# Optimization experiments

Hardware: AMD Instinct MI355X
Metric: run time of the kernel (lower is better)

## Reference

```python
import jax, jax.numpy as jnp
import numpy as np

N = 25600          # total nodes
B = 64             # graphs in batch
NPG = N // B       # nodes per graph (400)
K = 16             # in-degree (regular graph)
E = N * K          # edges
D = 128            # hidden dim = out dim
L = 4              # DGN layers
NUM_ATOM = 128


def _linear_init(key, out_s, in_s):
    lim = 1.0 / np.sqrt(in_s)
    return jax.random.uniform(key, (out_s, in_s), jnp.float32, -lim, lim)


def setup_inputs() -> dict:
    key = jax.random.key(0)
    ks = jax.random.split(key, 16)
    node_feat = jax.random.randint(ks[0], (N,), 0, NUM_ATOM)
    # K-regular in-degree graph, edges intra-graph; dst sorted
    dst = jnp.repeat(jnp.arange(N), K)                       # [E]
    src_local = jax.random.randint(ks[1], (E,), 0, NPG)
    src = (dst // NPG) * NPG + src_local                     # same graph as dst
    eig = jax.random.normal(ks[2], (E, 2), jnp.float32)
    snorm_n = jnp.full((N, 1), 1.0 / np.sqrt(NPG), jnp.float32)
    graph_ids = jnp.arange(N) // NPG
    emb = jax.random.normal(ks[3], (NUM_ATOM, D), jnp.float32) * 0.02
    pre_W = jnp.stack([_linear_init(jax.random.fold_in(ks[4], i), D, 2 * D) for i in range(L)])
    pre_b = jnp.zeros((L, D), jnp.float32)
    post_W = jnp.stack([_linear_init(jax.random.fold_in(ks[5], i), D, 5 * D) for i in range(L)])
    post_b = jnp.zeros((L, D), jnp.float32)
    r_W0 = _linear_init(ks[6], 64, 128); r_b0 = jnp.zeros((64,), jnp.float32)
    r_W1 = _linear_init(ks[7], 32, 64);  r_b1 = jnp.zeros((32,), jnp.float32)
    r_W2 = _linear_init(ks[8], 128, 32); r_b2 = jnp.zeros((128,), jnp.float32)
    return dict(node_feat=node_feat, src=src, dst=dst, eig=eig, snorm_n=snorm_n,
                graph_ids=graph_ids, emb=emb, pre_W=pre_W, pre_b=pre_b,
                post_W=post_W, post_b=post_b, r_W0=r_W0, r_b0=r_b0,
                r_W1=r_W1, r_b1=r_b1, r_W2=r_W2, r_b2=r_b2)


def _dgn_layer(h, src, dst, eig, snorm_n, Wp, bp, Wq, bq):
    n = h.shape[0]
    # pretrans on edges: Linear(cat(h_src, h_dst))  [E, D]
    z2 = jnp.concatenate([h[src], h[dst]], axis=-1)
    e = jnp.einsum('ei,oi->eo', z2, Wp) + bp
    seg_sum = lambda v: jax.ops.segment_sum(v, dst, num_segments=n, indices_are_sorted=True)
    s = seg_sum(e)
    mean = s / K
    mx = jax.ops.segment_max(e, dst, num_segments=n, indices_are_sorted=True)
    # directional aggregator (eig_idx=1)
    w = eig[:, 1]
    denom = seg_sum(jnp.abs(w)) + 1e-8                       # [n]
    ew = w / denom[dst]                                      # [E]
    dir_agg = jnp.abs(seg_sum(e * ew[:, None]) - seg_sum(ew)[:, None] * h)
    agg = jnp.concatenate([h, mean, s, mx, dir_agg], axis=-1)  # [n, 5D]
    hn = jnp.einsum('ni,oi->no', agg, Wq) + bq
    hn = hn * snorm_n           # graph_norm
    hn = jax.nn.relu(hn)
    return h + hn               # residual (in_dim == out_dim)


def reference(node_feat, src, dst, eig, snorm_n, graph_ids, emb,
              pre_W, pre_b, post_W, post_b,
              r_W0, r_b0, r_W1, r_b1, r_W2, r_b2):
    h = emb[node_feat]                                       # AtomEncoder
    for i in range(L):
        h = _dgn_layer(h, src, dst, eig, snorm_n, pre_W[i], pre_b[i], post_W[i], post_b[i])
    # mean_nodes per graph (equal-sized graphs)
    hg = jax.ops.segment_sum(h, graph_ids, num_segments=B, indices_are_sorted=True) / NPG
    y = jax.nn.relu(hg @ r_W0.T + r_b0)
    y = jax.nn.relu(y @ r_W1.T + r_b1)
    return y @ r_W2.T + r_b2                                 # [B, 128]
```

## Files before the change

kernel.cpp:

```cpp
#include <hip/hip_runtime.h>
#include <cstddef>

#define NN 25600
#define BB 64
#define NPG 400
#define KK 16
#define LL 4

typedef _Float16 half_t;
typedef _Float16 h8 __attribute__((ext_vector_type(8)));
typedef _Float16 h4 __attribute__((ext_vector_type(4)));
typedef _Float16 h2 __attribute__((ext_vector_type(2)));
typedef float f32x4 __attribute__((ext_vector_type(4)));

__global__ __launch_bounds__(256) void prep_k(const float* __restrict__ preW,
                                              const float* __restrict__ preb,
                                              const float* __restrict__ postW,
                                              half_t* __restrict__ WpreH,
                                              half_t* __restrict__ WpreL,
                                              float* __restrict__ bpre,
                                              half_t* __restrict__ WpostH,
                                              half_t* __restrict__ WpostL) {
  int idx = blockIdx.x * 256 + threadIdx.x;
  const int n1 = LL * 256 * 128;
  const int n2 = n1 + LL * 256;
  const int n3 = n2 + LL * 128 * 512;
  if (idx < n1) {
    int l = idx / 32768;
    int q = idx % 32768;
    int j = q & 7, lane = (q >> 3) & 63, kc = (q >> 9) & 3, c16 = q >> 11;
    int col = c16 * 16 + (lane & 15);
    int k = kc * 32 + (lane >> 4) * 8 + j;
    float v = (col < 128) ? preW[(size_t)l * 32768 + (size_t)col * 256 + k]
                          : preW[(size_t)l * 32768 + (size_t)(col - 128) * 256 + 128 + k];
    half_t hi = (half_t)v;
    WpreH[idx] = hi;
    WpreL[idx] = (half_t)(v - (float)hi);
  } else if (idx < n2) {
    int r = idx - n1;
    int l = r / 256, o = r % 256;
    bpre[r] = (o < 128) ? 0.f : preb[l * 128 + (o - 128)];
  } else if (idx < n3) {
    int r = idx - n2;
    int l = r / 65536;
    int q = r % 65536;
    int j = q & 7, lane = (q >> 3) & 63, kc = (q >> 9) & 15, c16 = q >> 13;
    int col = c16 * 16 + (lane & 15);
    int k = kc * 32 + (lane >> 4) * 8 + j;
    int jblk = k >> 7, kk = k & 127;
    const float* base = postW + (size_t)l * 128 * 640 + (size_t)col * 640;
    float v;
    if (jblk == 0)      v = base[kk];
    else if (jblk == 1) v = base[128 + kk] * (1.f / 16.f) + base[256 + kk];
    else if (jblk == 2) v = base[384 + kk];
    else                v = base[512 + kk];
    half_t hi = (half_t)v;
    WpostH[r] = hi;
    WpostL[r] = (half_t)(v - (float)hi);
  }
}

__global__ __launch_bounds__(256) void embed_k(const int* __restrict__ nf,
                                               const float* __restrict__ emb,
                                               half_t* __restrict__ Hh,
                                               half_t* __restrict__ Hl) {
  int idx = blockIdx.x * 256 + threadIdx.x;
  int n = idx >> 5;
  int d4 = idx & 31;
  int a = nf[n];
  float4 v = *(const float4*)(emb + (size_t)a * 128 + d4 * 4);
  h4 hi, lo;
  const float* vp = &v.x;
#pragma unroll
  for (int j = 0; j < 4; ++j) {
    half_t h = (half_t)vp[j];
    hi[j] = h;
    lo[j] = (half_t)(vp[j] - (float)h);
  }
  *(h4*)(Hh + (size_t)n * 128 + d4 * 4) = hi;
  *(h4*)(Hl + (size_t)n * 128 + d4 * 4) = lo;
}

__global__ __launch_bounds__(256) void pre_gemm_k(const half_t* __restrict__ Ah_g,
                                                  const half_t* __restrict__ Al_g,
                                                  const half_t* __restrict__ Wh_g,
                                                  const half_t* __restrict__ Wl_g,
                                                  float* __restrict__ preA) {
  __shared__ half_t Ahs[64][132];
  __shared__ half_t Als[64][132];
  const int tid = threadIdx.x;
  const int bid = blockIdx.x;
  const int swz = (bid & 7) * 50 + (bid >> 3);
  const int r0 = swz * 64;
  const int wid = tid >> 6, lane = tid & 63;
  const int wm = wid >> 1, wn = wid & 1;
  const int lr = lane & 15, lk = (lane >> 4) * 8;
  f32x4 acc[2][4] = {};

  {
    const int row = tid >> 2;
#pragma unroll
    for (int s = 0; s < 4; ++s) {
      const int koff = (tid & 3) * 8 + s * 32;
      const size_t g = (size_t)(r0 + row) * 128 + koff;
      *(h8*)&Ahs[row][koff] = *(const h8*)(Ah_g + g);
      *(h8*)&Als[row][koff] = *(const h8*)(Al_g + g);
    }
  }
  __syncthreads();

#pragma unroll
  for (int kc = 0; kc < 4; ++kc) {
    h8 af[2][2];
#pragma unroll
    for (int mi = 0; mi < 2; ++mi) {
      const int r = wm * 32 + mi * 16 + lr;
      af[mi][0] = *(const h8*)&Ahs[r][kc * 32 + lk];
      af[mi][1] = *(const h8*)&Als[r][kc * 32 + lk];
    }
#pragma unroll
    for (int nj = 0; nj < 4; ++nj) {
      const size_t fi = ((size_t)((wn * 4 + nj) * 4 + kc) * 64 + lane) * 8;
      const h8 b0v = *(const h8*)(Wh_g + fi);
      const h8 b1v = *(const h8*)(Wl_g + fi);
#pragma unroll
      for (int mi = 0; mi < 2; ++mi) {
        acc[mi][nj] = __builtin_amdgcn_mfma_f32_16x16x32_f16(af[mi][0], b0v, acc[mi][nj], 0, 0, 0);
        acc[mi][nj] = __builtin_amdgcn_mfma_f32_16x16x32_f16(af[mi][0], b1v, acc[mi][nj], 0, 0, 0);
        acc[mi][nj] = __builtin_amdgcn_mfma_f32_16x16x32_f16(af[mi][1], b0v, acc[mi][nj], 0, 0, 0);
      }
    }
  }
#pragma unroll
  for (int mi = 0; mi < 2; ++mi) {
    const int rowb = r0 + wm * 32 + mi * 16 + (lane >> 4) * 4;
#pragma unroll
    for (int nj = 0; nj < 4; ++nj) {
      const int col = wn * 64 + nj * 16 + lr;
#pragma unroll
      for (int q = 0; q < 4; ++q) {
        preA[(size_t)(rowb + q) * 128 + col] = acc[mi][nj][q];
      }
    }
  }
}

__global__ __launch_bounds__(256) void agg_post_k(const float* __restrict__ preA,
                                                  const int* __restrict__ src,
                                                  const float* __restrict__ eig,
                                                  const half_t* __restrict__ WpHg,
                                                  const half_t* __restrict__ WpLg,
                                                  const float* __restrict__ bpre128,
                                                  half_t* __restrict__ Hh,
                                                  half_t* __restrict__ Hl,
                                                  const half_t* __restrict__ Wh,
                                                  const half_t* __restrict__ Wl,
                                                  const float* __restrict__ bias,
                                                  const float* __restrict__ snorm) {
  __shared__ half_t Ah[16][392];
  __shared__ half_t Al[16][392];
  __shared__ float bsh[16][132];
  const int tid = threadIdx.x;
  const int bid = blockIdx.x;
  const int swz = (bid & 7) * 200 + (bid >> 3);
  const int r0 = swz * 16;
  const int wid = tid >> 6, lane = tid & 63;
  const int wn = wid;
  const int lr = lane & 15, lk = (lane >> 4) * 8;
  const int d0 = 2 * lane;

  const int frow = r0 + lr;
  h8 afh[4][2];
#pragma unroll
  for (int hc = 0; hc < 4; ++hc) {
    afh[hc][0] = *(const h8*)(Hh + (size_t)frow * 128 + hc * 32 + lk);
    afh[hc][1] = *(const h8*)(Hl + (size_t)frow * 128 + hc * 32 + lk);
  }

  {
    f32x4 bacc[2] = {};
#pragma unroll
    for (int kc = 0; kc < 4; ++kc) {
#pragma unroll
      for (int nj = 0; nj < 2; ++nj) {
        const size_t fi = ((size_t)((8 + wn * 2 + nj) * 4 + kc) * 64 + lane) * 8;
        const h8 b0v = *(const h8*)(WpHg + fi);
        const h8 b1v = *(const h8*)(WpLg + fi);
        bacc[nj] = __builtin_amdgcn_mfma_f32_16x16x32_f16(afh[kc][0], b0v, bacc[nj], 0, 0, 0);
        bacc[nj] = __builtin_amdgcn_mfma_f32_16x16x32_f16(afh[kc][0], b1v, bacc[nj], 0, 0, 0);
        bacc[nj] = __builtin_amdgcn_mfma_f32_16x16x32_f16(afh[kc][1], b0v, bacc[nj], 0, 0, 0);
      }
    }
    const int rowb = (lane >> 4) * 4;
#pragma unroll
    for (int nj = 0; nj < 2; ++nj) {
      const int col = (wn * 2 + nj) * 16 + lr;
      const float bv = bpre128[col];
#pragma unroll
      for (int q = 0; q < 4; ++q) {
        bsh[rowb + q][col] = bacc[nj][q] + bv;
      }
    }
  }
  __syncthreads();

  for (int i = 0; i < 4; ++i) {
    const int lrow = wid * 4 + i;
    const int n = r0 + lrow;
    int sv[KK];
    float wv[KK];
    {
      const int4* sp4 = (const int4*)(src + (size_t)n * KK);
      const float4* ep4 = (const float4*)(eig + (size_t)n * KK * 2);
#pragma unroll
      for (int t = 0; t < 4; ++t) {
        const int4 s4 = sp4[t];
        sv[4 * t + 0] = s4.x;
        sv[4 * t + 1] = s4.y;
        sv[4 * t + 2] = s4.z;
        sv[4 * t + 3] = s4.w;
      }
#pragma unroll
      for (int t = 0; t < 8; ++t) {
        const float4 e4 = ep4[t];
        wv[2 * t + 0] = e4.y;
        wv[2 * t + 1] = e4.w;
      }
    }
    float denom = 0.f;
#pragma unroll
    for (int e = 0; e < KK; ++e) denom += fabsf(wv[e]);
    denom += 1e-8f;
    const float inv = 1.f / denom;
    float sum_ew = 0.f;
#pragma unroll
    for (int e = 0; e < KK; ++e) {
      wv[e] *= inv;
      sum_ew += wv[e];
    }
    float sA0 = 0.f, sA1 = 0.f, wA0 = 0.f, wA1 = 0.f;
    float mA0 = -3.402823466e+38f, mA1 = -3.402823466e+38f;
#pragma unroll
    for (int e = 0; e < KK; ++e) {
      const float2 a = *(const float2*)(preA + (size_t)sv[e] * 128 + d0);
      sA0 += a.x;
      sA1 += a.y;
      wA0 = fmaf(wv[e], a.x, wA0);
      wA1 = fmaf(wv[e], a.y, wA1);
      mA0 = fmaxf(mA0, a.x);
      mA1 = fmaxf(mA1, a.y);
    }
    const float2 b = {bsh[lrow][d0], bsh[lrow][d0 + 1]};
    const h2 hh2 = *(const h2*)(Hh + (size_t)n * 128 + d0);
    const h2 hl2 = *(const h2*)(Hl + (size_t)n * 128 + d0);
    const float hx = (float)hh2[0] + (float)hl2[0];
    const float hy = (float)hh2[1] + (float)hl2[1];
    auto wr2 = [&](int kcol, float v0, float v1) {
      h2 hi, lo;
      hi[0] = (half_t)v0;
      hi[1] = (half_t)v1;
      lo[0] = (half_t)(v0 - (float)hi[0]);
      lo[1] = (half_t)(v1 - (float)hi[1]);
      *(h2*)&Ah[lrow][kcol] = hi;
      *(h2*)&Al[lrow][kcol] = lo;
    };
    wr2(d0, sA0 + 16.f * b.x, sA1 + 16.f * b.y);
    wr2(128 + d0, mA0 + b.x, mA1 + b.y);
    wr2(256 + d0, fabsf(wA0 + sum_ew * (b.x - hx)), fabsf(wA1 + sum_ew * (b.y - hy)));
  }
  __syncthreads();

  f32x4 acc[2] = {};
#pragma unroll
  for (int kc = 0; kc < 16; ++kc) {
    h8 a0, a1;
    if (kc < 4) {
      a0 = afh[kc & 3][0];
      a1 = afh[kc & 3][1];
    } else {
      a0 = *(const h8*)&Ah[lr][(kc - 4) * 32 + lk];
      a1 = *(const h8*)&Al[lr][(kc - 4) * 32 + lk];
    }
#pragma unroll
    for (int nj = 0; nj < 2; ++nj) {
      const size_t fi = ((size_t)((wn * 2 + nj) * 16 + kc) * 64 + lane) * 8;
      const h8 b0v = *(const h8*)(Wh + fi);
      const h8 b1v = *(const h8*)(Wl + fi);
      acc[nj] = __builtin_amdgcn_mfma_f32_16x16x32_f16(a0, b0v, acc[nj], 0, 0, 0);
      acc[nj] = __builtin_amdgcn_mfma_f32_16x16x32_f16(a0, b1v, acc[nj], 0, 0, 0);
      acc[nj] = __builtin_amdgcn_mfma_f32_16x16x32_f16(a1, b0v, acc[nj], 0, 0, 0);
    }
  }

  const int rowb = r0 + (lane >> 4) * 4;
#pragma unroll
  for (int nj = 0; nj < 2; ++nj) {
    const int col = wn * 32 + nj * 16 + lr;
    const float bv = bias[col];
#pragma unroll
    for (int q = 0; q < 4; ++q) {
      const int r = rowb + q;
      float a = acc[nj][q] + bv;
      a *= snorm[r];
      a = fmaxf(a, 0.f);
      const size_t off = (size_t)r * 128 + col;
      const float hold = (float)Hh[off] + (float)Hl[off];
      const float hn = hold + a;
      const half_t hi = (half_t)hn;
      Hh[off] = hi;
      Hl[off] = (half_t)(hn - (float)hi);
    }
  }
}

__global__ __launch_bounds__(256) void reduce_mlp_k(const half_t* __restrict__ Hh,
                                                    const half_t* __restrict__ Hl,
                                                    const float* __restrict__ W0, const float* __restrict__ b0,
                                                    const float* __restrict__ W1, const float* __restrict__ b1,
                                                    const float* __restrict__ W2, const float* __restrict__ b2,
                                                    float* __restrict__ out) {
  __shared__ float hgs[128];
  __shared__ float red[128];
  __shared__ float y0s[64];
  __shared__ float y1s[32];
  __shared__ float wb[64 * 130];
  const int g = blockIdx.x;
  const int t = threadIdx.x;
  {
    const int d = t & 127, hf = t >> 7;
    const size_t base = ((size_t)g * NPG + (size_t)hf * 200) * 128 + d;
    float acc = 0.f;
    for (int i = 0; i < 200; ++i) {
      const size_t off = base + (size_t)i * 128;
      acc += (float)Hh[off] + (float)Hl[off];
    }
    if (hf) red[d] = acc;
    __syncthreads();
    if (!hf) hgs[d] = (acc + red[d]) * (1.f / (float)NPG);
  }
  __syncthreads();
  for (int idx = t; idx < 64 * 128; idx += 256) {
    wb[(idx >> 7) * 130 + (idx & 127)] = W0[idx];
  }
  __syncthreads();
  if (t < 64) {
    float a = b0[t];
    const float* w = &wb[t * 130];
    for (int k = 0; k < 128; ++k) a = fmaf(hgs[k], w[k], a);
    y0s[t] = fmaxf(a, 0.f);
  }
  __syncthreads();
  for (int idx = t; idx < 32 * 64; idx += 256) {
    wb[(idx >> 6) * 66 + (idx & 63)] = W1[idx];
  }
  __syncthreads();
  if (t < 32) {
    float a = b1[t];
    const float* w = &wb[t * 66];
    for (int k = 0; k < 64; ++k) a = fmaf(y0s[k], w[k], a);
    y1s[t] = fmaxf(a, 0.f);
  }
  __syncthreads();
  for (int idx = t; idx < 128 * 32; idx += 256) {
    wb[(idx >> 5) * 34 + (idx & 31)] = W2[idx];
  }
  __syncthreads();
  if (t < 128) {
    float a = b2[t];
    const float* w = &wb[t * 34];
    for (int k = 0; k < 32; ++k) a = fmaf(y1s[k], w[k], a);
    out[(size_t)g * 128 + t] = a;
  }
}

extern "C" void kernel_launch(void* const* d_in, const int* in_sizes, int n_in,
                              void* d_out, int out_size, void* d_ws, size_t ws_size,
                              hipStream_t stream) {
  const int* node_feat = (const int*)d_in[0];
  const int* src = (const int*)d_in[1];
  const float* eig = (const float*)d_in[3];
  const float* snorm = (const float*)d_in[4];
  const float* emb = (const float*)d_in[6];
  const float* preW = (const float*)d_in[7];
  const float* preb = (const float*)d_in[8];
  const float* postW = (const float*)d_in[9];
  const float* postb = (const float*)d_in[10];
  const float* rW0 = (const float*)d_in[11];
  const float* rb0 = (const float*)d_in[12];
  const float* rW1 = (const float*)d_in[13];
  const float* rb1 = (const float*)d_in[14];
  const float* rW2 = (const float*)d_in[15];
  const float* rb2 = (const float*)d_in[16];
  float* out = (float*)d_out;

  half_t* Hh = (half_t*)d_ws;
  half_t* Hl = Hh + (size_t)NN * 128;
  float* preA = (float*)(Hl + (size_t)NN * 128);
  half_t* WpreH = (half_t*)(preA + (size_t)NN * 128);
  half_t* WpreL = WpreH + (size_t)LL * 32768;
  half_t* WpostH = WpreL + (size_t)LL * 32768;
  half_t* WpostL = WpostH + (size_t)LL * 65536;
  float* bpre = (float*)(WpostL + (size_t)LL * 65536);

  prep_k<<<1540, 256, 0, stream>>>(preW, preb, postW, WpreH, WpreL, bpre, WpostH, WpostL);
  embed_k<<<(NN * 32) / 256, 256, 0, stream>>>(node_feat, emb, Hh, Hl);

  for (int l = 0; l < LL; ++l) {
    pre_gemm_k<<<NN / 64, 256, 0, stream>>>(
        Hh, Hl, WpreH + (size_t)l * 32768, WpreL + (size_t)l * 32768, preA);
    agg_post_k<<<NN / 16, 256, 0, stream>>>(
        preA, src, eig,
        WpreH + (size_t)l * 32768, WpreL + (size_t)l * 32768,
        bpre + (size_t)l * 256 + 128,
        Hh, Hl,
        WpostH + (size_t)l * 65536, WpostL + (size_t)l * 65536,
        postb + (size_t)l * 128, snorm);
  }

  reduce_mlp_k<<<BB, 256, 0, stream>>>(Hh, Hl, rW0, rb0, rW1, rb1, rW2, rb2, out);
}
```

Measured before the change: 280.1 us.

## Double row tile in agg_post and stream neighbor gathers via global_load_lds

The aggregation+post-GEMM kernel now processes 32 rows per block instead of 16, so each weight fragment loaded from global memory is reused across two MFMA row tiles, and the grid is halved. The per-edge gather of preA rows is rewritten to use global_load_lds into a per-wave double-buffered LDS stage, with explicit vmcnt/lgkmcnt waits so the next pair of neighbor rows loads while the current pair is accumulated. This targets gather latency and weight-load traffic, at the cost of more LDS per block, more registers, fewer blocks, and fragile hand-written waitcnt ordering.

```diff
diff --git a/kernel.cpp b/kernel.cpp
--- a/kernel.cpp
+++ b/kernel.cpp
@@ -12,6 +12,9 @@
 typedef _Float16 h4 __attribute__((ext_vector_type(4)));
 typedef _Float16 h2 __attribute__((ext_vector_type(2)));
 typedef float f32x4 __attribute__((ext_vector_type(4)));
+
+#define GCAST(p) ((const __attribute__((address_space(1))) void*)(p))
+#define SCAST(p) ((__attribute__((address_space(3))) void*)(p))
 
 __global__ __launch_bounds__(256) void prep_k(const float* __restrict__ preW,
                                               const float* __restrict__ preb,
@@ -145,40 +148,46 @@
   }
 }
 
-__global__ __launch_bounds__(256) void agg_post_k(const float* __restrict__ preA,
-                                                  const int* __restrict__ src,
-                                                  const float* __restrict__ eig,
-                                                  const half_t* __restrict__ WpHg,
-                                                  const half_t* __restrict__ WpLg,
-                                                  const float* __restrict__ bpre128,
-                                                  half_t* __restrict__ Hh,
-                                                  half_t* __restrict__ Hl,
-                                                  const half_t* __restrict__ Wh,
-                                                  const half_t* __restrict__ Wl,
-                                                  const float* __restrict__ bias,
-                                                  const float* __restrict__ snorm) {
-  __shared__ half_t Ah[16][392];
-  __shared__ half_t Al[16][392];
-  __shared__ float bsh[16][132];
+__global__ __launch_bounds__(256, 2) void agg_post_k(const float* __restrict__ preA,
+                                                     const int* __restrict__ src,
+                                                     const float* __restrict__ eig,
+                                                     const half_t* __restrict__ WpHg,
+                                                     const half_t* __restrict__ WpLg,
+                                                     const float* __restrict__ bpre128,
+                                                     half_t* __restrict__ Hh,
+                                                     half_t* __restrict__ Hl,
+                                                     const half_t* __restrict__ Wh,
+                                                     const half_t* __restrict__ Wl,
+                                                     const float* __restrict__ bias,
+                                                     const float* __restrict__ snorm) {
+  __shared__ half_t Ah[32][392];
+  __shared__ half_t Al[32][392];
+  __shared__ float bsh[32][132];
+  __shared__ float stage[4][2][2][128];
   const int tid = threadIdx.x;
   const int bid = blockIdx.x;
-  const int swz = (bid & 7) * 200 + (bid >> 3);
-  const int r0 = swz * 16;
+  const int swz = (bid & 7) * 100 + (bid >> 3);
+  const int r0 = swz * 32;
   const int wid = tid >> 6, lane = tid & 63;
   const int wn = wid;
   const int lr = lane & 15, lk = (lane >> 4) * 8;
   const int d0 = 2 * lane;
-
-  const int frow = r0 + lr;
-  h8 afh[4][2];
-#pragma unroll
-  for (int hc = 0; hc < 4; ++hc) {
-    afh[hc][0] = *(const h8*)(Hh + (size_t)frow * 128 + hc * 32 + lk);
-    afh[hc][1] = *(const h8*)(Hl + (size_t)frow * 128 + hc * 32 + lk);
+  const int glane4 = (lane & 31) * 4;
+  const int gsel = lane >> 5;
+
+  h8 afh[2][4][2];
+#pragma unroll
+  for (int mi = 0; mi < 2; ++mi) {
+    const int frow = r0 + mi * 16 + lr;
+#pragma unroll
+    for (int hc = 0; hc < 4; ++hc) {
+      afh[mi][hc][0] = *(const h8*)(Hh + (size_t)frow * 128 + hc * 32 + lk);
+      afh[mi][hc][1] = *(const h8*)(Hl + (size_t)frow * 128 + hc * 32 + lk);
+    }
   }
 
   {
-    f32x4 bacc[2] = {};
+    f32x4 bacc[2][2] = {};
 #pragma unroll
     for (int kc = 0; kc < 4; ++kc) {
 #pragma unroll
@@ -186,26 +195,32 @@
         const size_t fi = ((size_t)((8 + wn * 2 + nj) * 4 + kc) * 64 + lane) * 8;
         const h8 b0v = *(const h8*)(WpHg + fi);
         const h8 b1v = *(const h8*)(WpLg + fi);
-        bacc[nj] = __builtin_amdgcn_mfma_f32_16x16x32_f16(afh[kc][0], b0v, bacc[nj], 0, 0, 0);
-        bacc[nj] = __builtin_amdgcn_mfma_f32_16x16x32_f16(afh[kc][0], b1v, bacc[nj], 0, 0, 0);
-        bacc[nj] = __builtin_amdgcn_mfma_f32_16x16x32_f16(afh[kc][1], b0v, bacc[nj], 0, 0, 0);
+#pragma unroll
+        for (int mi = 0; mi < 2; ++mi) {
+          bacc[mi][nj] = __builtin_amdgcn_mfma_f32_16x16x32_f16(afh[mi][kc][0], b0v, bacc[mi][nj], 0, 0, 0);
+          bacc[mi][nj] = __builtin_amdgcn_mfma_f32_16x16x32_f16(afh[mi][kc][0], b1v, bacc[mi][nj], 0, 0, 0);
+          bacc[mi][nj] = __builtin_amdgcn_mfma_f32_16x16x32_f16(afh[mi][kc][1], b0v, bacc[mi][nj], 0, 0, 0);
+        }
       }
     }
     const int rowb = (lane >> 4) * 4;
 #pragma unroll
-    for (int nj = 0; nj < 2; ++nj) {
-      const int col = (wn * 2 + nj) * 16 + lr;
-      const float bv = bpre128[col];
-#pragma unroll
-      for (int q = 0; q < 4; ++q) {
-        bsh[rowb + q][col] = bacc[nj][q] + bv;
-      }
-    }
-  }
-  __syncthreads();
-
-  for (int i = 0; i < 4; ++i) {
-    const int lrow = wid * 4 + i;
+    for (int mi = 0; mi < 2; ++mi) {
+#pragma unroll
+      for (int nj = 0; nj < 2; ++nj) {
+        const int col = (wn * 2 + nj) * 16 + lr;
+        const float bv = bpre128[col];
+#pragma unroll
+        for (int q = 0; q < 4; ++q) {
+          bsh[mi * 16 + rowb + q][col] = bacc[mi][nj][q] + bv;
+        }
+      }
+    }
+  }
+  __syncthreads();
+
+  for (int i = 0; i < 8; ++i) {
+    const int lrow = wid * 8 + i;
     const int n = r0 + lrow;
     int sv[KK];
     float wv[KK];
@@ -227,6 +242,14 @@
         wv[2 * t + 1] = e4.w;
       }
     }
+    const h2 hh2 = *(const h2*)(Hh + (size_t)n * 128 + d0);
+    const h2 hl2 = *(const h2*)(Hl + (size_t)n * 128 + d0);
+    const float hx = (float)hh2[0] + (float)hl2[0];
+    const float hy = (float)hh2[1] + (float)hl2[1];
+    const float bx = bsh[lrow][d0];
+    const float by = bsh[lrow][d0 + 1];
+    const float tbx = bx - hx;
+    const float tby = by - hy;
     float denom = 0.f;
 #pragma unroll
     for (int e = 0; e < KK; ++e) denom += fabsf(wv[e]);
@@ -238,23 +261,45 @@
       wv[e] *= inv;
       sum_ew += wv[e];
     }
-    float sA0 = 0.f, sA1 = 0.f, wA0 = 0.f, wA1 = 0.f;
-    float mA0 = -3.402823466e+38f, mA1 = -3.402823466e+38f;
-#pragma unroll
-    for (int e = 0; e < KK; ++e) {
-      const float2 a = *(const float2*)(preA + (size_t)sv[e] * 128 + d0);
-      sA0 += a.x;
-      sA1 += a.y;
-      wA0 = fmaf(wv[e], a.x, wA0);
-      wA1 = fmaf(wv[e], a.y, wA1);
-      mA0 = fmaxf(mA0, a.x);
-      mA1 = fmaxf(mA1, a.y);
-    }
-    const float2 b = {bsh[lrow][d0], bsh[lrow][d0 + 1]};
-    const h2 hh2 = *(const h2*)(Hh + (size_t)n * 128 + d0);
-    const h2 hl2 = *(const h2*)(Hl + (size_t)n * 128 + d0);
-    const float hx = (float)hh2[0] + (float)hl2[0];
-    const float hy = (float)hh2[1] + (float)hl2[1];
+    float sX = 0.f, sY = 0.f, wX = 0.f, wY = 0.f;
+    float mX = -3.402823466e+38f, mY = -3.402823466e+38f;
+
+#define ISSUE(c, buf)                                                              \
+    {                                                                              \
+      const float* gp = preA + (size_t)sv[2 * (c) + gsel] * 128 + glane4;          \
+      __builtin_amdgcn_global_load_lds(GCAST(gp), SCAST(&stage[wid][buf][0][0]),   \
+                                       16, 0, 0);                                  \
+    }
+#define ACCUM(c, buf)                                                              \
+    {                                                                              \
+      const float2 aA = *(const float2*)&stage[wid][buf][0][d0];                   \
+      const float2 aB = *(const float2*)&stage[wid][buf][1][d0];                   \
+      sX += aA.x; sY += aA.y;                                                      \
+      wX = fmaf(wv[2 * (c)], aA.x, wX); wY = fmaf(wv[2 * (c)], aA.y, wY);          \
+      mX = fmaxf(mX, aA.x); mY = fmaxf(mY, aA.y);                                  \
+      sX += aB.x; sY += aB.y;                                                      \
+      wX = fmaf(wv[2 * (c) + 1], aB.x, wX); wY = fmaf(wv[2 * (c) + 1], aB.y, wY);  \
+      mX = fmaxf(mX, aB.x); mY = fmaxf(mY, aB.y);                                  \
+    }
+#define WAITV1 asm volatile("s_waitcnt vmcnt(1)" ::: "memory");
+#define WAITV0 asm volatile("s_waitcnt vmcnt(0)" ::: "memory");
+#define LGKM0  asm volatile("s_waitcnt lgkmcnt(0)" ::: "memory");
+
+    ISSUE(0, 0) ISSUE(1, 1)
+    WAITV1 ACCUM(0, 0) LGKM0 ISSUE(2, 0)
+    WAITV1 ACCUM(1, 1) LGKM0 ISSUE(3, 1)
+    WAITV1 ACCUM(2, 0) LGKM0 ISSUE(4, 0)
+    WAITV1 ACCUM(3, 1) LGKM0 ISSUE(5, 1)
+    WAITV1 ACCUM(4, 0) LGKM0 ISSUE(6, 0)
+    WAITV1 ACCUM(5, 1) LGKM0 ISSUE(7, 1)
+    WAITV1 ACCUM(6, 0)
+    WAITV0 ACCUM(7, 1)
+#undef ISSUE
+#undef ACCUM
+#undef WAITV1
+#undef WAITV0
+#undef LGKM0
+
     auto wr2 = [&](int kcol, float v0, float v1) {
       h2 hi, lo;
       hi[0] = (half_t)v0;
@@ -264,51 +309,60 @@
       *(h2*)&Ah[lrow][kcol] = hi;
       *(h2*)&Al[lrow][kcol] = lo;
     };
-    wr2(d0, sA0 + 16.f * b.x, sA1 + 16.f * b.y);
-    wr2(128 + d0, mA0 + b.x, mA1 + b.y);
-    wr2(256 + d0, fabsf(wA0 + sum_ew * (b.x - hx)), fabsf(wA1 + sum_ew * (b.y - hy)));
-  }
-  __syncthreads();
-
-  f32x4 acc[2] = {};
+    wr2(d0, sX + 16.f * bx, sY + 16.f * by);
+    wr2(128 + d0, mX + bx, mY + by);
+    wr2(256 + d0, fabsf(wX + sum_ew * tbx), fabsf(wY + sum_ew * tby));
+  }
+  __syncthreads();
+
+  f32x4 acc[2][2] = {};
 #pragma unroll
   for (int kc = 0; kc < 16; ++kc) {
-    h8 a0, a1;
-    if (kc < 4) {
-      a0 = afh[kc & 3][0];
-      a1 = afh[kc & 3][1];
-    } else {
-      a0 = *(const h8*)&Ah[lr][(kc - 4) * 32 + lk];
-      a1 = *(const h8*)&Al[lr][(kc - 4) * 32 + lk];
+    h8 a0[2], a1[2];
+#pragma unroll
+    for (int mi = 0; mi < 2; ++mi) {
+      if (kc < 4) {
+        a0[mi] = afh[mi][kc & 3][0];
+        a1[mi] = afh[mi][kc & 3][1];
+      } else {
+        a0[mi] = *(const h8*)&Ah[mi * 16 + lr][(kc - 4) * 32 + lk];
+        a1[mi] = *(const h8*)&Al[mi * 16 + lr][(kc - 4) * 32 + lk];
+      }
     }
 #pragma unroll
     for (int nj = 0; nj < 2; ++nj) {
       const size_t fi = ((size_t)((wn * 2 + nj) * 16 + kc) * 64 + lane) * 8;
       const h8 b0v = *(const h8*)(Wh + fi);
       const h8 b1v = *(const h8*)(Wl + fi);
-      acc[nj] = __builtin_amdgcn_mfma_f32_16x16x32_f16(a0, b0v, acc[nj], 0, 0, 0);
-      acc[nj] = __builtin_amdgcn_mfma_f32_16x16x32_f16(a0, b1v, acc[nj], 0, 0, 0);
-      acc[nj] = __builtin_amdgcn_mfma_f32_16x16x32_f16(a1, b0v, acc[nj], 0, 0, 0);
-    }
-  }
-
-  const int rowb = r0 + (lane >> 4) * 4;
-#pragma unroll
-  for (int nj = 0; nj < 2; ++nj) {
-    const int col = wn * 32 + nj * 16 + lr;
-    const float bv = bias[col];
-#pragma unroll
-    for (int q = 0; q < 4; ++q) {
-      const int r = rowb + q;
-      float a = acc[nj][q] + bv;
-      a *= snorm[r];
-      a = fmaxf(a, 0.f);
-      const size_t off = (size_t)r * 128 + col;
-      const float hold = (float)Hh[off] + (float)Hl[off];
-      const float hn = hold + a;
-      const half_t hi = (half_t)hn;
-      Hh[off] = hi;
-      Hl[off] = (half_t)(hn - (float)hi);
+#pragma unroll
+      for (int mi = 0; mi < 2; ++mi) {
+        acc[mi][nj] = __builtin_amdgcn_mfma_f32_16x16x32_f16(a0[mi], b0v, acc[mi][nj], 0, 0, 0);
+        acc[mi][nj] = __builtin_amdgcn_mfma_f32_16x16x32_f16(a0[mi], b1v, acc[mi][nj], 0, 0, 0);
+        acc[mi][nj] = __builtin_amdgcn_mfma_f32_16x16x32_f16(a1[mi], b0v, acc[mi][nj], 0, 0, 0);
+      }
+    }
+  }
+
+#pragma unroll
+  for (int mi = 0; mi < 2; ++mi) {
+    const int rowb = r0 + mi * 16 + (lane >> 4) * 4;
+#pragma unroll
+    for (int nj = 0; nj < 2; ++nj) {
+      const int col = wn * 32 + nj * 16 + lr;
+      const float bv = bias[col];
+#pragma unroll
+      for (int q = 0; q < 4; ++q) {
+        const int r = rowb + q;
+        float a = acc[mi][nj][q] + bv;
+        a *= snorm[r];
+        a = fmaxf(a, 0.f);
+        const size_t off = (size_t)r * 128 + col;
+        const float hold = (float)Hh[off] + (float)Hl[off];
+        const float hn = hold + a;
+        const half_t hi = (half_t)hn;
+        Hh[off] = hi;
+        Hl[off] = (half_t)(hn - (float)hi);
+      }
     }
   }
 }
@@ -408,7 +462,7 @@
   for (int l = 0; l < LL; ++l) {
     pre_gemm_k<<<NN / 64, 256, 0, stream>>>(
         Hh, Hl, WpreH + (size_t)l * 32768, WpreL + (size_t)l * 32768, preA);
-    agg_post_k<<<NN / 16, 256, 0, stream>>>(
+    agg_post_k<<<NN / 32, 256, 0, stream>>>(
         preA, src, eig,
         WpreH + (size_t)l * 32768, WpreL + (size_t)l * 32768,
         bpre + (size_t)l * 256 + 128,
```

Measured after the change: 297.7 us. 1.06x slower.

## Split fused aggregate+post kernel into batched GEMM, gather, and post-GEMM stages

Applied to the files above, without the earlier changes.

Restructures each layer from two kernels into three. A 3-slab GEMM computes the src projection, the dst projection with bias, and the h-part of the post linear with bias in one launch. A one-warp-per-node gather kernel then writes sum, max and directional aggregates to a float staging buffer, and a swizzled-LDS post GEMM over the remaining 384 input columns adds the precomputed h contribution. The aim is more parallelism and larger MFMA tiles than the old 16-row fused kernel, in exchange for extra global round trips through a 384-wide fp32 Agg buffer and a postC buffer.

```diff
diff --git a/kernel.cpp b/kernel.cpp
--- a/kernel.cpp
+++ b/kernel.cpp
@@ -14,49 +14,46 @@
 typedef float f32x4 __attribute__((ext_vector_type(4)));
 
 __global__ __launch_bounds__(256) void prep_k(const float* __restrict__ preW,
-                                              const float* __restrict__ preb,
                                               const float* __restrict__ postW,
-                                              half_t* __restrict__ WpreH,
-                                              half_t* __restrict__ WpreL,
-                                              float* __restrict__ bpre,
-                                              half_t* __restrict__ WpostH,
-                                              half_t* __restrict__ WpostL) {
-  int idx = blockIdx.x * 256 + threadIdx.x;
-  const int n1 = LL * 256 * 128;
-  const int n2 = n1 + LL * 256;
-  const int n3 = n2 + LL * 128 * 512;
+                                              half_t* __restrict__ Wk1H,
+                                              half_t* __restrict__ Wk1L,
+                                              half_t* __restrict__ WaggH,
+                                              half_t* __restrict__ WaggL) {
+  const int idx = blockIdx.x * 256 + threadIdx.x;
+  const int n1 = LL * 3 * 16384;
   if (idx < n1) {
-    int l = idx / 32768;
-    int q = idx % 32768;
-    int j = q & 7, lane = (q >> 3) & 63, kc = (q >> 9) & 3, c16 = q >> 11;
+    int l = idx / 49152;
+    int q = idx % 49152;
+    int slab = q / 16384;
+    int qq = q & 16383;
+    int j = qq & 7, lane = (qq >> 3) & 63, kc = (qq >> 9) & 3, c16 = qq >> 11;
     int col = c16 * 16 + (lane & 15);
     int k = kc * 32 + (lane >> 4) * 8 + j;
-    float v = (col < 128) ? preW[(size_t)l * 32768 + (size_t)col * 256 + k]
-                          : preW[(size_t)l * 32768 + (size_t)(col - 128) * 256 + 128 + k];
+    float v;
+    if (slab == 0)      v = preW[(size_t)l * 32768 + (size_t)col * 256 + k];
+    else if (slab == 1) v = preW[(size_t)l * 32768 + (size_t)col * 256 + 128 + k];
+    else                v = postW[(size_t)l * 81920 + (size_t)col * 640 + k];
     half_t hi = (half_t)v;
-    WpreH[idx] = hi;
-    WpreL[idx] = (half_t)(v - (float)hi);
-  } else if (idx < n2) {
+    Wk1H[idx] = hi;
+    Wk1L[idx] = (half_t)(v - (float)hi);
+  } else if (idx < 2 * n1) {
     int r = idx - n1;
-    int l = r / 256, o = r % 256;
-    bpre[r] = (o < 128) ? 0.f : preb[l * 128 + (o - 128)];
-  } else if (idx < n3) {
-    int r = idx - n2;
-    int l = r / 65536;
-    int q = r % 65536;
-    int j = q & 7, lane = (q >> 3) & 63, kc = (q >> 9) & 15, c16 = q >> 13;
+    int l = r / 49152;
+    int q = r % 49152;
+    int c16 = q / 6144;
+    int rr = q % 6144;
+    int kc = rr >> 9, lane = (rr >> 3) & 63, j = rr & 7;
     int col = c16 * 16 + (lane & 15);
     int k = kc * 32 + (lane >> 4) * 8 + j;
-    int jblk = k >> 7, kk = k & 127;
-    const float* base = postW + (size_t)l * 128 * 640 + (size_t)col * 640;
+    int kk = k & 127, jb = k >> 7;
+    const float* base = postW + (size_t)l * 81920 + (size_t)col * 640;
     float v;
-    if (jblk == 0)      v = base[kk];
-    else if (jblk == 1) v = base[128 + kk] * (1.f / 16.f) + base[256 + kk];
-    else if (jblk == 2) v = base[384 + kk];
-    else                v = base[512 + kk];
+    if (jb == 0)      v = base[128 + kk] * (1.f / 16.f) + base[256 + kk];
+    else if (jb == 1) v = base[384 + kk];
+    else              v = base[512 + kk];
     half_t hi = (half_t)v;
-    WpostH[r] = hi;
-    WpostL[r] = (half_t)(v - (float)hi);
+    WaggH[r] = hi;
+    WaggL[r] = (half_t)(v - (float)hi);
   }
 }
 
@@ -81,15 +78,20 @@
   *(h4*)(Hl + (size_t)n * 128 + d4 * 4) = lo;
 }
 
-__global__ __launch_bounds__(256) void pre_gemm_k(const half_t* __restrict__ Ah_g,
-                                                  const half_t* __restrict__ Al_g,
-                                                  const half_t* __restrict__ Wh_g,
-                                                  const half_t* __restrict__ Wl_g,
-                                                  float* __restrict__ preA) {
+__global__ __launch_bounds__(256) void gemm3_k(const half_t* __restrict__ Ah_g,
+                                               const half_t* __restrict__ Al_g,
+                                               const half_t* __restrict__ WH,
+                                               const half_t* __restrict__ WL,
+                                               const float* __restrict__ biasB,
+                                               const float* __restrict__ biasP,
+                                               float* __restrict__ preA,
+                                               float* __restrict__ Agg,
+                                               float* __restrict__ postC) {
   __shared__ half_t Ahs[64][132];
   __shared__ half_t Als[64][132];
   const int tid = threadIdx.x;
   const int bid = blockIdx.x;
+  const int y = blockIdx.y;
   const int swz = (bid & 7) * 50 + (bid >> 3);
   const int r0 = swz * 64;
   const int wid = tid >> 6, lane = tid & 63;
@@ -109,6 +111,8 @@
   }
   __syncthreads();
 
+  const half_t* WHs = WH + y * 16384;
+  const half_t* WLs = WL + y * 16384;
 #pragma unroll
   for (int kc = 0; kc < 4; ++kc) {
     h8 af[2][2];
@@ -121,8 +125,8 @@
 #pragma unroll
     for (int nj = 0; nj < 4; ++nj) {
       const size_t fi = ((size_t)((wn * 4 + nj) * 4 + kc) * 64 + lane) * 8;
-      const h8 b0v = *(const h8*)(Wh_g + fi);
-      const h8 b1v = *(const h8*)(Wl_g + fi);
+      const h8 b0v = *(const h8*)(WHs + fi);
+      const h8 b1v = *(const h8*)(WLs + fi);
 #pragma unroll
       for (int mi = 0; mi < 2; ++mi) {
         acc[mi][nj] = __builtin_amdgcn_mfma_f32_16x16x32_f16(af[mi][0], b0v, acc[mi][nj], 0, 0, 0);
@@ -137,178 +141,177 @@
 #pragma unroll
     for (int nj = 0; nj < 4; ++nj) {
       const int col = wn * 64 + nj * 16 + lr;
-#pragma unroll
-      for (int q = 0; q < 4; ++q) {
-        preA[(size_t)(rowb + q) * 128 + col] = acc[mi][nj][q];
+      if (y == 0) {
+#pragma unroll
+        for (int q = 0; q < 4; ++q)
+          preA[(size_t)(rowb + q) * 128 + col] = acc[mi][nj][q];
+      } else if (y == 1) {
+        const float bv = biasB[col];
+#pragma unroll
+        for (int q = 0; q < 4; ++q)
+          Agg[(size_t)(rowb + q) * 384 + col] = acc[mi][nj][q] + bv;
+      } else {
+        const float bv = biasP[col];
+        f32x4 v = acc[mi][nj];
+        v[0] += bv; v[1] += bv; v[2] += bv; v[3] += bv;
+        const int rowtile = swz * 4 + wm * 2 + mi;
+        *(f32x4*)&postC[((size_t)(rowtile * 8 + wn * 4 + nj) * 64 + lane) * 4] = v;
       }
     }
   }
 }
 
-__global__ __launch_bounds__(256) void agg_post_k(const float* __restrict__ preA,
-                                                  const int* __restrict__ src,
-                                                  const float* __restrict__ eig,
-                                                  const half_t* __restrict__ WpHg,
-                                                  const half_t* __restrict__ WpLg,
-                                                  const float* __restrict__ bpre128,
-                                                  half_t* __restrict__ Hh,
-                                                  half_t* __restrict__ Hl,
-                                                  const half_t* __restrict__ Wh,
-                                                  const half_t* __restrict__ Wl,
-                                                  const float* __restrict__ bias,
-                                                  const float* __restrict__ snorm) {
-  __shared__ half_t Ah[16][392];
-  __shared__ half_t Al[16][392];
-  __shared__ float bsh[16][132];
+__global__ __launch_bounds__(256) void agg_k(const float* __restrict__ preA,
+                                             const int* __restrict__ src,
+                                             const float* __restrict__ eig,
+                                             const half_t* __restrict__ Hh,
+                                             const half_t* __restrict__ Hl,
+                                             float* __restrict__ Agg) {
+  const int bid = blockIdx.x;
+  const int swz = (bid & 7) * 800 + (bid >> 3);
+  const int wid = threadIdx.x >> 6, lane = threadIdx.x & 63;
+  const int n = swz * 4 + wid;
+  const int d0 = 2 * lane;
+  int sv[KK];
+  float wv[KK];
+  {
+    const int4* sp4 = (const int4*)(src + (size_t)n * KK);
+    const float4* ep4 = (const float4*)(eig + (size_t)n * KK * 2);
+#pragma unroll
+    for (int t = 0; t < 4; ++t) {
+      const int4 s4 = sp4[t];
+      sv[4 * t + 0] = s4.x; sv[4 * t + 1] = s4.y;
+      sv[4 * t + 2] = s4.z; sv[4 * t + 3] = s4.w;
+    }
+#pragma unroll
+    for (int t = 0; t < 8; ++t) {
+      const float4 e4 = ep4[t];
+      wv[2 * t + 0] = e4.y; wv[2 * t + 1] = e4.w;
+    }
+  }
+  const float2 b = *(const float2*)(Agg + (size_t)n * 384 + d0);
+  const h2 hh2 = *(const h2*)(Hh + (size_t)n * 128 + d0);
+  const h2 hl2 = *(const h2*)(Hl + (size_t)n * 128 + d0);
+  const float hx = (float)hh2[0] + (float)hl2[0];
+  const float hy = (float)hh2[1] + (float)hl2[1];
+  float denom = 0.f;
+#pragma unroll
+  for (int e = 0; e < KK; ++e) denom += fabsf(wv[e]);
+  denom += 1e-8f;
+  const float inv = 1.f / denom;
+  float sum_ew = 0.f;
+#pragma unroll
+  for (int e = 0; e < KK; ++e) {
+    wv[e] *= inv;
+    sum_ew += wv[e];
+  }
+  float sX = 0.f, sY = 0.f, wX = 0.f, wY = 0.f;
+  float mX = -3.402823466e+38f, mY = -3.402823466e+38f;
+#pragma unroll
+  for (int e = 0; e < KK; ++e) {
+    const float2 a = *(const float2*)(preA + (size_t)sv[e] * 128 + d0);
+    sX += a.x; sY += a.y;
+    wX = fmaf(wv[e], a.x, wX); wY = fmaf(wv[e], a.y, wY);
+    mX = fmaxf(mX, a.x); mY = fmaxf(mY, a.y);
+  }
+  float* row = Agg + (size_t)n * 384;
+  *(float2*)(row + d0) = {sX + 16.f * b.x, sY + 16.f * b.y};
+  *(float2*)(row + 128 + d0) = {mX + b.x, mY + b.y};
+  *(float2*)(row + 256 + d0) = {fabsf(wX + sum_ew * (b.x - hx)),
+                                fabsf(wY + sum_ew * (b.y - hy))};
+}
+
+__global__ __launch_bounds__(256) void aggpost_k(const float* __restrict__ Agg,
+                                                 const float* __restrict__ postC,
+                                                 const half_t* __restrict__ WH,
+                                                 const half_t* __restrict__ WL,
+                                                 const float* __restrict__ snorm,
+                                                 half_t* __restrict__ Hh,
+                                                 half_t* __restrict__ Hl) {
+  __shared__ half_t AhS[32 * 384];
+  __shared__ half_t AlS[32 * 384];
   const int tid = threadIdx.x;
   const int bid = blockIdx.x;
-  const int swz = (bid & 7) * 200 + (bid >> 3);
-  const int r0 = swz * 16;
+  const int swz = (bid & 7) * 100 + (bid >> 3);
+  const int r0 = swz * 32;
   const int wid = tid >> 6, lane = tid & 63;
   const int wn = wid;
-  const int lr = lane & 15, lk = (lane >> 4) * 8;
-  const int d0 = 2 * lane;
-
-  const int frow = r0 + lr;
-  h8 afh[4][2];
-#pragma unroll
-  for (int hc = 0; hc < 4; ++hc) {
-    afh[hc][0] = *(const h8*)(Hh + (size_t)frow * 128 + hc * 32 + lk);
-    afh[hc][1] = *(const h8*)(Hl + (size_t)frow * 128 + hc * 32 + lk);
-  }
-
-  {
-    f32x4 bacc[2] = {};
-#pragma unroll
-    for (int kc = 0; kc < 4; ++kc) {
-#pragma unroll
-      for (int nj = 0; nj < 2; ++nj) {
-        const size_t fi = ((size_t)((8 + wn * 2 + nj) * 4 + kc) * 64 + lane) * 8;
-        const h8 b0v = *(const h8*)(WpHg + fi);
-        const h8 b1v = *(const h8*)(WpLg + fi);
-        bacc[nj] = __builtin_amdgcn_mfma_f32_16x16x32_f16(afh[kc][0], b0v, bacc[nj], 0, 0, 0);
-        bacc[nj] = __builtin_amdgcn_mfma_f32_16x16x32_f16(afh[kc][0], b1v, bacc[nj], 0, 0, 0);
-        bacc[nj] = __builtin_amdgcn_mfma_f32_16x16x32_f16(afh[kc][1], b0v, bacc[nj], 0, 0, 0);
+  const int lr = lane & 15, ksub = lane >> 4;
+
+#pragma unroll
+  for (int it = 0; it < 12; ++it) {
+    const int id = it * 256 + tid;
+    const int r = id / 96, c = id % 96;
+    const float4 v = *(const float4*)(Agg + (size_t)(r0 + r) * 384 + c * 4);
+    h4 hi, lo;
+    const float* vp = &v.x;
+#pragma unroll
+    for (int j = 0; j < 4; ++j) {
+      half_t h = (half_t)vp[j];
+      hi[j] = h;
+      lo[j] = (half_t)(vp[j] - (float)h);
+    }
+    const int g8 = (c >> 1) ^ (r & 7);
+    const int dst = r * 384 + (g8 << 3) + ((c & 1) << 2);
+    *(h4*)&AhS[dst] = hi;
+    *(h4*)&AlS[dst] = lo;
+  }
+  __syncthreads();
+
+  f32x4 acc[2][2];
+#pragma unroll
+  for (int mi = 0; mi < 2; ++mi) {
+    const int rowtile = swz * 2 + mi;
+#pragma unroll
+    for (int nj = 0; nj < 2; ++nj) {
+      acc[mi][nj] = *(const f32x4*)&postC[((size_t)(rowtile * 8 + wn * 2 + nj) * 64 + lane) * 4];
+    }
+  }
+
+#pragma unroll
+  for (int kc = 0; kc < 12; ++kc) {
+    h8 a0[2], a1[2];
+#pragma unroll
+    for (int mi = 0; mi < 2; ++mi) {
+      const int row = mi * 16 + lr;
+      const int cl = kc * 4 + ksub;
+      const int off = row * 384 + ((cl ^ (lr & 7)) << 3);
+      a0[mi] = *(const h8*)&AhS[off];
+      a1[mi] = *(const h8*)&AlS[off];
+    }
+#pragma unroll
+    for (int nj = 0; nj < 2; ++nj) {
+      const size_t fi = ((size_t)((wn * 2 + nj) * 12 + kc) * 64 + lane) * 8;
+      const h8 b0v = *(const h8*)(WH + fi);
+      const h8 b1v = *(const h8*)(WL + fi);
+#pragma unroll
+      for (int mi = 0; mi < 2; ++mi) {
+        acc[mi][nj] = __builtin_amdgcn_mfma_f32_16x16x32_f16(a0[mi], b0v, acc[mi][nj], 0, 0, 0);
+        acc[mi][nj] = __builtin_amdgcn_mfma_f32_16x16x32_f16(a0[mi], b1v, acc[mi][nj], 0, 0, 0);
+        acc[mi][nj] = __builtin_amdgcn_mfma_f32_16x16x32_f16(a1[mi], b0v, acc[mi][nj], 0, 0, 0);
       }
     }
-    const int rowb = (lane >> 4) * 4;
+  }
+
+#pragma unroll
+  for (int mi = 0; mi < 2; ++mi) {
+    const int rowb = r0 + mi * 16 + (lane >> 4) * 4;
 #pragma unroll
     for (int nj = 0; nj < 2; ++nj) {
-      const int col = (wn * 2 + nj) * 16 + lr;
-      const float bv = bpre128[col];
+      const int col = wn * 32 + nj * 16 + lr;
 #pragma unroll
       for (int q = 0; q < 4; ++q) {
-        bsh[rowb + q][col] = bacc[nj][q] + bv;
+        const int r = rowb + q;
+        float a = acc[mi][nj][q];
+        a *= snorm[r];
+        a = fmaxf(a, 0.f);
+        const size_t off = (size_t)r * 128 + col;
+        const float hold = (float)Hh[off] + (float)Hl[off];
+        const float hn = hold + a;
+        const half_t hi = (half_t)hn;
+        Hh[off] = hi;
+        Hl[off] = (half_t)(hn - (float)hi);
       }
-    }
-  }
-  __syncthreads();
-
-  for (int i = 0; i < 4; ++i) {
-    const int lrow = wid * 4 + i;
-    const int n = r0 + lrow;
-    int sv[KK];
-    float wv[KK];
-    {
-      const int4* sp4 = (const int4*)(src + (size_t)n * KK);
-      const float4* ep4 = (const float4*)(eig + (size_t)n * KK * 2);
-#pragma unroll
-      for (int t = 0; t < 4; ++t) {
-        const int4 s4 = sp4[t];
-        sv[4 * t + 0] = s4.x;
-        sv[4 * t + 1] = s4.y;
-        sv[4 * t + 2] = s4.z;
-        sv[4 * t + 3] = s4.w;
-      }
-#pragma unroll
-      for (int t = 0; t < 8; ++t) {
-        const float4 e4 = ep4[t];
-        wv[2 * t + 0] = e4.y;
-        wv[2 * t + 1] = e4.w;
-      }
-    }
-    float denom = 0.f;
-#pragma unroll
-    for (int e = 0; e < KK; ++e) denom += fabsf(wv[e]);
-    denom += 1e-8f;
-    const float inv = 1.f / denom;
-    float sum_ew = 0.f;
-#pragma unroll
-    for (int e = 0; e < KK; ++e) {
-      wv[e] *= inv;
-      sum_ew += wv[e];
-    }
-    float sA0 = 0.f, sA1 = 0.f, wA0 = 0.f, wA1 = 0.f;
-    float mA0 = -3.402823466e+38f, mA1 = -3.402823466e+38f;
-#pragma unroll
-    for (int e = 0; e < KK; ++e) {
-      const float2 a = *(const float2*)(preA + (size_t)sv[e] * 128 + d0);
-      sA0 += a.x;
-      sA1 += a.y;
-      wA0 = fmaf(wv[e], a.x, wA0);
-      wA1 = fmaf(wv[e], a.y, wA1);
-      mA0 = fmaxf(mA0, a.x);
-      mA1 = fmaxf(mA1, a.y);
-    }
-    const float2 b = {bsh[lrow][d0], bsh[lrow][d0 + 1]};
-    const h2 hh2 = *(const h2*)(Hh + (size_t)n * 128 + d0);
-    const h2 hl2 = *(const h2*)(Hl + (size_t)n * 128 + d0);
-    const float hx = (float)hh2[0] + (float)hl2[0];
-    const float hy = (float)hh2[1] + (float)hl2[1];
-    auto wr2 = [&](int kcol, float v0, float v1) {
-      h2 hi, lo;
-      hi[0] = (half_t)v0;
-      hi[1] = (half_t)v1;
-      lo[0] = (half_t)(v0 - (float)hi[0]);
-      lo[1] = (half_t)(v1 - (float)hi[1]);
-      *(h2*)&Ah[lrow][kcol] = hi;
-      *(h2*)&Al[lrow][kcol] = lo;
-    };
-    wr2(d0, sA0 + 16.f * b.x, sA1 + 16.f * b.y);
-    wr2(128 + d0, mA0 + b.x, mA1 + b.y);
-    wr2(256 + d0, fabsf(wA0 + sum_ew * (b.x - hx)), fabsf(wA1 + sum_ew * (b.y - hy)));
-  }
-  __syncthreads();
-
-  f32x4 acc[2] = {};
-#pragma unroll
-  for (int kc = 0; kc < 16; ++kc) {
-    h8 a0, a1;
-    if (kc < 4) {
-      a0 = afh[kc & 3][0];
-      a1 = afh[kc & 3][1];
-    } else {
-      a0 = *(const h8*)&Ah[lr][(kc - 4) * 32 + lk];
-      a1 = *(const h8*)&Al[lr][(kc - 4) * 32 + lk];
-    }
-#pragma unroll
-    for (int nj = 0; nj < 2; ++nj) {
-      const size_t fi = ((size_t)((wn * 2 + nj) * 16 + kc) * 64 + lane) * 8;
-      const h8 b0v = *(const h8*)(Wh + fi);
-      const h8 b1v = *(const h8*)(Wl + fi);
-      acc[nj] = __builtin_amdgcn_mfma_f32_16x16x32_f16(a0, b0v, acc[nj], 0, 0, 0);
-      acc[nj] = __builtin_amdgcn_mfma_f32_16x16x32_f16(a0, b1v, acc[nj], 0, 0, 0);
-      acc[nj] = __builtin_amdgcn_mfma_f32_16x16x32_f16(a1, b0v, acc[nj], 0, 0, 0);
-    }
-  }
-
-  const int rowb = r0 + (lane >> 4) * 4;
-#pragma unroll
-  for (int nj = 0; nj < 2; ++nj) {
-    const int col = wn * 32 + nj * 16 + lr;
-    const float bv = bias[col];
-#pragma unroll
-    for (int q = 0; q < 4; ++q) {
-      const int r = rowb + q;
-      float a = acc[nj][q] + bv;
-      a *= snorm[r];
-      a = fmaxf(a, 0.f);
-      const size_t off = (size_t)r * 128 + col;
-      const float hold = (float)Hh[off] + (float)Hl[off];
-      const float hn = hold + a;
-      const half_t hi = (half_t)hn;
-      Hh[off] = hi;
-      Hl[off] = (half_t)(hn - (float)hi);
     }
   }
 }
@@ -396,25 +399,25 @@
   half_t* Hh = (half_t*)d_ws;
   half_t* Hl = Hh + (size_t)NN * 128;
   float* preA = (float*)(Hl + (size_t)NN * 128);
-  half_t* WpreH = (half_t*)(preA + (size_t)NN * 128);
-  half_t* WpreL = WpreH + (size_t)LL * 32768;
-  half_t* WpostH = WpreL + (size_t)LL * 32768;
-  half_t* WpostL = WpostH + (size_t)LL * 65536;
-  float* bpre = (float*)(WpostL + (size_t)LL * 65536);
-
-  prep_k<<<1540, 256, 0, stream>>>(preW, preb, postW, WpreH, WpreL, bpre, WpostH, WpostL);
+  float* Agg = preA + (size_t)NN * 128;
+  float* postC = Agg + (size_t)NN * 384;
+  half_t* Wk1H = (half_t*)(postC + (size_t)NN * 128);
+  half_t* Wk1L = Wk1H + (size_t)LL * 49152;
+  half_t* WaggH = Wk1L + (size_t)LL * 49152;
+  half_t* WaggL = WaggH + (size_t)LL * 49152;
+
+  prep_k<<<1536, 256, 0, stream>>>(preW, postW, Wk1H, Wk1L, WaggH, WaggL);
   embed_k<<<(NN * 32) / 256, 256, 0, stream>>>(node_feat, emb, Hh, Hl);
 
   for (int l = 0; l < LL; ++l) {
-    pre_gemm_k<<<NN / 64, 256, 0, stream>>>(
-        Hh, Hl, WpreH + (size_t)l * 32768, WpreL + (size_t)l * 32768, preA);
-    agg_post_k<<<NN / 16, 256, 0, stream>>>(
-        preA, src, eig,
-        WpreH + (size_t)l * 32768, WpreL + (size_t)l * 32768,
-        bpre + (size_t)l * 256 + 128,
-        Hh, Hl,
-        WpostH + (size_t)l * 65536, WpostL + (size_t)l * 65536,
-        postb + (size_t)l * 128, snorm);
+    gemm3_k<<<dim3(400, 3), 256, 0, stream>>>(
+        Hh, Hl, Wk1H + (size_t)l * 49152, Wk1L + (size_t)l * 49152,
+        preb + (size_t)l * 128, postb + (size_t)l * 128,
+        preA, Agg, postC);
+    agg_k<<<NN / 4, 256, 0, stream>>>(preA, src, eig, Hh, Hl, Agg);
+    aggpost_k<<<NN / 32, 256, 0, stream>>>(
+        Agg, postC, WaggH + (size_t)l * 49152, WaggL + (size_t)l * 49152,
+        snorm, Hh, Hl);
   }
 
   reduce_mlp_k<<<BB, 256, 0, stream>>>(Hh, Hl, rW0, rb0, rW1, rb1, rW2, rb2, out);
```

After: 315.4 us. +12.6%, slower.

## Store pre-activations as split fp16 and gather neighbors via global_load_lds staging

Applied to the files above, without the earlier changes.

The pre-transform GEMM now writes its output as fp16 hi/lo pairs instead of fp32. The aggregation kernel gathers neighbor rows with direct global-to-LDS loads, 8 edges at a time into a per-wave staging buffer, then reads them back from LDS. It also adds a launch-bounds occupancy hint of 2 blocks. Byte volume stays about the same, but the gathers become 16-byte full-row loads instead of scattered float2 reads. The cost is extra LDS traffic, explicit waitcnt serialization between the two halves, and narrow scalar half stores in the GEMM epilogue.

```diff
diff --git a/kernel.cpp b/kernel.cpp
--- a/kernel.cpp
+++ b/kernel.cpp
@@ -12,6 +12,9 @@
 typedef _Float16 h4 __attribute__((ext_vector_type(4)));
 typedef _Float16 h2 __attribute__((ext_vector_type(2)));
 typedef float f32x4 __attribute__((ext_vector_type(4)));
+
+#define GCAST(p) ((const __attribute__((address_space(1))) void*)(p))
+#define SCAST(p) ((__attribute__((address_space(3))) void*)(p))
 
 __global__ __launch_bounds__(256) void prep_k(const float* __restrict__ preW,
                                               const float* __restrict__ preb,
@@ -85,7 +88,8 @@
                                                   const half_t* __restrict__ Al_g,
                                                   const half_t* __restrict__ Wh_g,
                                                   const half_t* __restrict__ Wl_g,
-                                                  float* __restrict__ preA) {
+                                                  half_t* __restrict__ preAh,
+                                                  half_t* __restrict__ preAl) {
   __shared__ half_t Ahs[64][132];
   __shared__ half_t Als[64][132];
   const int tid = threadIdx.x;
@@ -139,27 +143,34 @@
       const int col = wn * 64 + nj * 16 + lr;
 #pragma unroll
       for (int q = 0; q < 4; ++q) {
-        preA[(size_t)(rowb + q) * 128 + col] = acc[mi][nj][q];
-      }
-    }
-  }
-}
-
-__global__ __launch_bounds__(256) void agg_post_k(const float* __restrict__ preA,
-                                                  const int* __restrict__ src,
-                                                  const float* __restrict__ eig,
-                                                  const half_t* __restrict__ WpHg,
-                                                  const half_t* __restrict__ WpLg,
-                                                  const float* __restrict__ bpre128,
-                                                  half_t* __restrict__ Hh,
-                                                  half_t* __restrict__ Hl,
-                                                  const half_t* __restrict__ Wh,
-                                                  const half_t* __restrict__ Wl,
-                                                  const float* __restrict__ bias,
-                                                  const float* __restrict__ snorm) {
+        const float v = acc[mi][nj][q];
+        const half_t hi = (half_t)v;
+        const size_t off = (size_t)(rowb + q) * 128 + col;
+        preAh[off] = hi;
+        preAl[off] = (half_t)(v - (float)hi);
+      }
+    }
+  }
+}
+
+__global__ __launch_bounds__(256, 2) void agg_post_k(const half_t* __restrict__ preAh,
+                                                     const half_t* __restrict__ preAl,
+                                                     const int* __restrict__ src,
+                                                     const float* __restrict__ eig,
+                                                     const half_t* __restrict__ WpHg,
+                                                     const half_t* __restrict__ WpLg,
+                                                     const float* __restrict__ bpre128,
+                                                     half_t* __restrict__ Hh,
+                                                     half_t* __restrict__ Hl,
+                                                     const half_t* __restrict__ Wh,
+                                                     const half_t* __restrict__ Wl,
+                                                     const float* __restrict__ bias,
+                                                     const float* __restrict__ snorm) {
   __shared__ half_t Ah[16][392];
   __shared__ half_t Al[16][392];
   __shared__ float bsh[16][132];
+  __shared__ half_t stageH[4][8][128];
+  __shared__ half_t stageL[4][8][128];
   const int tid = threadIdx.x;
   const int bid = blockIdx.x;
   const int swz = (bid & 7) * 200 + (bid >> 3);
@@ -168,6 +179,8 @@
   const int wn = wid;
   const int lr = lane & 15, lk = (lane >> 4) * 8;
   const int d0 = 2 * lane;
+  const int grow4 = lane >> 4;
+  const int gcol8 = (lane & 15) * 8;
 
   const int frow = r0 + lr;
   h8 afh[4][2];
@@ -227,6 +240,15 @@
         wv[2 * t + 1] = e4.w;
       }
     }
+    asm volatile("s_waitcnt lgkmcnt(0)" ::: "memory");
+    __builtin_amdgcn_global_load_lds(GCAST(preAh + (size_t)sv[0 + grow4] * 128 + gcol8),
+                                     SCAST(&stageH[wid][0][0]), 16, 0, 0);
+    __builtin_amdgcn_global_load_lds(GCAST(preAh + (size_t)sv[4 + grow4] * 128 + gcol8),
+                                     SCAST(&stageH[wid][4][0]), 16, 0, 0);
+    __builtin_amdgcn_global_load_lds(GCAST(preAl + (size_t)sv[0 + grow4] * 128 + gcol8),
+                                     SCAST(&stageL[wid][0][0]), 16, 0, 0);
+    __builtin_amdgcn_global_load_lds(GCAST(preAl + (size_t)sv[4 + grow4] * 128 + gcol8),
+                                     SCAST(&stageL[wid][4][0]), 16, 0, 0);
     float denom = 0.f;
 #pragma unroll
     for (int e = 0; e < KK; ++e) denom += fabsf(wv[e]);
@@ -240,15 +262,43 @@
     }
     float sA0 = 0.f, sA1 = 0.f, wA0 = 0.f, wA1 = 0.f;
     float mA0 = -3.402823466e+38f, mA1 = -3.402823466e+38f;
-#pragma unroll
-    for (int e = 0; e < KK; ++e) {
-      const float2 a = *(const float2*)(preA + (size_t)sv[e] * 128 + d0);
-      sA0 += a.x;
-      sA1 += a.y;
-      wA0 = fmaf(wv[e], a.x, wA0);
-      wA1 = fmaf(wv[e], a.y, wA1);
-      mA0 = fmaxf(mA0, a.x);
-      mA1 = fmaxf(mA1, a.y);
+    asm volatile("s_waitcnt vmcnt(0)" ::: "memory");
+#pragma unroll
+    for (int e = 0; e < 8; ++e) {
+      const h2 ah2 = *(const h2*)&stageH[wid][e][d0];
+      const h2 al2 = *(const h2*)&stageL[wid][e][d0];
+      const float ax = (float)ah2[0] + (float)al2[0];
+      const float ay = (float)ah2[1] + (float)al2[1];
+      sA0 += ax;
+      sA1 += ay;
+      wA0 = fmaf(wv[e], ax, wA0);
+      wA1 = fmaf(wv[e], ay, wA1);
+      mA0 = fmaxf(mA0, ax);
+      mA1 = fmaxf(mA1, ay);
+    }
+    asm volatile("s_waitcnt lgkmcnt(0)" ::: "memory");
+    __builtin_amdgcn_global_load_lds(GCAST(preAh + (size_t)sv[8 + grow4] * 128 + gcol8),
+                                     SCAST(&stageH[wid][0][0]), 16, 0, 0);
+    __builtin_amdgcn_global_load_lds(GCAST(preAh + (size_t)sv[12 + grow4] * 128 + gcol8),
+                                     SCAST(&stageH[wid][4][0]), 16, 0, 0);
+    __builtin_amdgcn_global_load_lds(GCAST(preAl + (size_t)sv[8 + grow4] * 128 + gcol8),
+                                     SCAST(&stageL[wid][0][0]), 16, 0, 0);
+    __builtin_amdgcn_global_load_lds(GCAST(preAl + (size_t)sv[12 + grow4] * 128 + gcol8),
+                                     SCAST(&stageL[wid][4][0]), 16, 0, 0);
+    asm volatile("s_waitcnt vmcnt(0)" ::: "memory");
+#pragma unroll
+    for (int e = 0; e < 8; ++e) {
+      const h2 ah2 = *(const h2*)&stageH[wid][e][d0];
+      const h2 al2 = *(const h2*)&stageL[wid][e][d0];
+      const float ax = (float)ah2[0] + (float)al2[0];
+      const float ay = (float)ah2[1] + (float)al2[1];
+      const float w = wv[8 + e];
+      sA0 += ax;
+      sA1 += ay;
+      wA0 = fmaf(w, ax, wA0);
+      wA1 = fmaf(w, ay, wA1);
+      mA0 = fmaxf(mA0, ax);
+      mA1 = fmaxf(mA1, ay);
     }
     const float2 b = {bsh[lrow][d0], bsh[lrow][d0 + 1]};
     const h2 hh2 = *(const h2*)(Hh + (size_t)n * 128 + d0);
@@ -395,8 +445,9 @@
 
   half_t* Hh = (half_t*)d_ws;
   half_t* Hl = Hh + (size_t)NN * 128;
-  float* preA = (float*)(Hl + (size_t)NN * 128);
-  half_t* WpreH = (half_t*)(preA + (size_t)NN * 128);
+  half_t* preAh = Hl + (size_t)NN * 128;
+  half_t* preAl = preAh + (size_t)NN * 128;
+  half_t* WpreH = preAl + (size_t)NN * 128;
   half_t* WpreL = WpreH + (size_t)LL * 32768;
   half_t* WpostH = WpreL + (size_t)LL * 32768;
   half_t* WpostL = WpostH + (size_t)LL * 65536;
@@ -407,9 +458,9 @@
 
   for (int l = 0; l < LL; ++l) {
     pre_gemm_k<<<NN / 64, 256, 0, stream>>>(
-        Hh, Hl, WpreH + (size_t)l * 32768, WpreL + (size_t)l * 32768, preA);
+        Hh, Hl, WpreH + (size_t)l * 32768, WpreL + (size_t)l * 32768, preAh, preAl);
     agg_post_k<<<NN / 16, 256, 0, stream>>>(
-        preA, src, eig,
+        preAh, preAl, src, eig,
         WpreH + (size_t)l * 32768, WpreL + (size_t)l * 32768,
         bpre + (size_t)l * 256 + 128,
         Hh, Hl,
```

Measured after the change: 262.4 us. 6.3% less time.
